# Kernel tuning notes

Hardware: AMD Instinct MI355X
Metric: run time of the kernel (lower is better)

Reference implementation:

```python
import jax, jax.numpy as jnp
import numpy as np

S, B, D = 2048, 2, 768
H = 12
DK = D // H
DFF = 3072
EPS = 1e-5


def _layernorm(x, g, b):
    mu = jnp.mean(x, axis=-1, keepdims=True)
    var = jnp.mean(jnp.square(x - mu), axis=-1, keepdims=True)
    return (x - mu) * jax.lax.rsqrt(var + EPS) * g + b


def setup_inputs() -> dict:
    key = jax.random.key(0)
    ks = jax.random.split(key, 12)
    s = 0.02
    return {
        "x": jax.random.normal(ks[0], (S, B, D), jnp.float32),
        "wq": jax.random.normal(ks[1], (D, D), jnp.float32) * s,
        "bq": jnp.zeros((D,), jnp.float32),
        "wk": jax.random.normal(ks[2], (D, D), jnp.float32) * s,
        "bk": jnp.zeros((D,), jnp.float32),
        "wv": jax.random.normal(ks[3], (D, D), jnp.float32) * s,
        "bv": jnp.zeros((D,), jnp.float32),
        "wo": jax.random.normal(ks[4], (D, D), jnp.float32) * s,
        "bo": jnp.zeros((D,), jnp.float32),
        "g1": jnp.ones((D,), jnp.float32),
        "b1": jnp.zeros((D,), jnp.float32),
        "g2": jnp.ones((D,), jnp.float32),
        "b2": jnp.zeros((D,), jnp.float32),
        "w1": jax.random.normal(ks[5], (DFF, D), jnp.float32) * s,
        "bb1": jnp.zeros((DFF,), jnp.float32),
        "w2": jax.random.normal(ks[6], (D, DFF), jnp.float32) * s,
        "bb2": jnp.zeros((D,), jnp.float32),
    }


def reference(x, wq, bq, wk, bk, wv, bv, wo, bo, g1, b1, g2, b2, w1, bb1, w2, bb2):
    scale = 1.0 / np.sqrt(DK)
    # --- pre-norm MHA ---
    z = _layernorm(x, g1, b1)                      # [S,B,D]
    q = (z @ wq.T + bq).reshape(S, B, H, DK)
    k = (z @ wk.T + bk).reshape(S, B, H, DK)
    v = (z @ wv.T + bv).reshape(S, B, H, DK)
    scores = jnp.einsum('ibhd,jbhd->ijbh', q, k) * scale  # [S,S,B,H]
    attn = jax.nn.softmax(scores, axis=1)                  # softmax over keys
    ctx = jnp.einsum('ijbh,jbhd->ibhd', attn, v).reshape(S, B, D)
    a = ctx @ wo.T + bo
    x = x + a
    # --- pre-norm FFN (ELU) ---
    z = _layernorm(x, g2, b2)
    h = jax.nn.elu(z @ w1.T + bb1)
    a = h @ w2.T + bb2
    return x + a
```

## Files before the change

kernel.cpp:

```cpp
#include <hip/hip_runtime.h>
#include <hip/hip_bf16.h>
#include <math.h>

#define S_LEN   2048
#define B_SZ    2
#define D_MODEL 768
#define N_HEADS 12
#define DFF     3072
#define N_TOK   4096
#define EPS     1e-5f
#define QKV_N   2304
#define SLOG2E  0.18033688011112042f

typedef __attribute__((ext_vector_type(8))) short short8;
typedef __attribute__((ext_vector_type(4))) float f32x4;
typedef unsigned long long u64;
typedef unsigned short u16;
typedef unsigned u32;

__device__ __forceinline__ void gload16(const void* g, void* l) {
    __builtin_amdgcn_global_load_lds(
        (const __attribute__((address_space(1))) void*)g,
        (__attribute__((address_space(3))) void*)l, 16, 0, 0);
}
__device__ __forceinline__ u16 f2bf(float x) {
    union { float f; unsigned u; } c; c.f = x;
    unsigned r = c.u + 0x7FFF + ((c.u >> 16) & 1);
    return (u16)(r >> 16);
}
__device__ __forceinline__ float bf2f(u16 u) {
    union { unsigned u; float f; } c; c.u = ((unsigned)u) << 16; return c.f;
}
__device__ __forceinline__ float fast_exp2(float x) {
    float r; asm("v_exp_f32 %0, %1" : "=v"(r) : "v"(x)); return r;
}

__global__ __launch_bounds__(256) void cvt_all(
    const float* __restrict__ wq, const float* __restrict__ wk,
    const float* __restrict__ wv, const float* __restrict__ wo,
    const float* __restrict__ w1, const float* __restrict__ w2,
    u16* __restrict__ dst)
{
    const int W = 147456;
    int i = blockIdx.x * 256 + threadIdx.x;
    const float* src; int off;
    if      (i <     W) { src = wq; off = 0;     }
    else if (i < 2 * W) { src = wk; off = W;     }
    else if (i < 3 * W) { src = wv; off = 2 * W; }
    else if (i < 4 * W) { src = wo; off = 3 * W; }
    else if (i < 8 * W) { src = w1; off = 4 * W; }
    else                { src = w2; off = 8 * W; }
    float4 v = ((const float4*)src)[i - off];
    union { u16 u[4]; u64 ll; } o;
    o.u[0] = f2bf(v.x); o.u[1] = f2bf(v.y); o.u[2] = f2bf(v.z); o.u[3] = f2bf(v.w);
    ((u64*)dst)[i] = o.ll;
}

__global__ __launch_bounds__(256) void concat_bias(
    const float* __restrict__ bq, const float* __restrict__ bk,
    const float* __restrict__ bv, float* __restrict__ d)
{
    int i = blockIdx.x * 256 + threadIdx.x;
    if (i < 768) d[i] = bq[i];
    else if (i < 1536) d[i] = bk[i - 768];
    else d[i] = bv[i - 1536];
}

__global__ __launch_bounds__(256) void ln_kernel(
    const float* __restrict__ x, const float* __restrict__ g,
    const float* __restrict__ b, u16* __restrict__ z)
{
    int row = blockIdx.x;
    const float* xr = x + (size_t)row * D_MODEL;
    u16* zr = z + (size_t)row * D_MODEL;
    int t = threadIdx.x;
    float loc[3];
    float s1 = 0.f, s2 = 0.f;
#pragma unroll
    for (int i = 0; i < 3; ++i) {
        float v = xr[t + 256 * i];
        loc[i] = v; s1 += v; s2 += v * v;
    }
#pragma unroll
    for (int off = 32; off > 0; off >>= 1) {
        s1 += __shfl_down(s1, off);
        s2 += __shfl_down(s2, off);
    }
    __shared__ float r1[4], r2[4];
    __shared__ float mu_s, is_s;
    int wave = t >> 6, lane = t & 63;
    if (lane == 0) { r1[wave] = s1; r2[wave] = s2; }
    __syncthreads();
    if (t == 0) {
        float a = r1[0] + r1[1] + r1[2] + r1[3];
        float c = r2[0] + r2[1] + r2[2] + r2[3];
        float mu = a * (1.f / D_MODEL);
        float var = c * (1.f / D_MODEL) - mu * mu;
        mu_s = mu; is_s = rsqrtf(var + EPS);
    }
    __syncthreads();
    float mu = mu_s, istd = is_s;
#pragma unroll
    for (int i = 0; i < 3; ++i) {
        int c = t + 256 * i;
        zr[c] = f2bf((loc[i] - mu) * istd * g[c] + b[c]);
    }
}

__global__ __launch_bounds__(256) void ln_fuse(
    const float* __restrict__ x, const u16* __restrict__ p0,
    const u16* __restrict__ p1, const float* __restrict__ bres,
    const float* __restrict__ g, const float* __restrict__ b,
    float* __restrict__ xout, u16* __restrict__ z)
{
    int row = blockIdx.x;
    const float* xr = x + (size_t)row * D_MODEL;
    const u16* p0r = p0 + (size_t)row * D_MODEL;
    const u16* p1r = p1 + (size_t)row * D_MODEL;
    int t = threadIdx.x;
    float loc[3];
    float s1 = 0.f, s2 = 0.f;
#pragma unroll
    for (int i = 0; i < 3; ++i) {
        int c = t + 256 * i;
        float v = xr[c] + bf2f(p0r[c]) + bf2f(p1r[c]) + bres[c];
        loc[i] = v; s1 += v; s2 += v * v;
    }
#pragma unroll
    for (int off = 32; off > 0; off >>= 1) {
        s1 += __shfl_down(s1, off);
        s2 += __shfl_down(s2, off);
    }
    __shared__ float r1[4], r2[4];
    __shared__ float mu_s, is_s;
    int wave = t >> 6, lane = t & 63;
    if (lane == 0) { r1[wave] = s1; r2[wave] = s2; }
    __syncthreads();
    if (t == 0) {
        float a = r1[0] + r1[1] + r1[2] + r1[3];
        float c = r2[0] + r2[1] + r2[2] + r2[3];
        float mu = a * (1.f / D_MODEL);
        float var = c * (1.f / D_MODEL) - mu * mu;
        mu_s = mu; is_s = rsqrtf(var + EPS);
    }
    __syncthreads();
    float mu = mu_s, istd = is_s;
    float* xo = xout + (size_t)row * D_MODEL;
    u16* zr = z + (size_t)row * D_MODEL;
#pragma unroll
    for (int i = 0; i < 3; ++i) {
        int c = t + 256 * i;
        xo[c] = loc[i];
        zr[c] = f2bf((loc[i] - mu) * istd * g[c] + b[c]);
    }
}

template <int MODE>
__global__ __launch_bounds__(256) void gemm_mfma(
    const u16* __restrict__ A, const u16* __restrict__ W,
    const float* __restrict__ bias, void* __restrict__ outp,
    u16* __restrict__ vt, int Ncols, int K, int lda, int ldw, int koff)
{
    __shared__ short AsB[3][128 * 32];
    __shared__ short BsB[3][128 * 32];

    const int t = threadIdx.x;
    const int lane = t & 63, w = t >> 6;
    const int wr = w >> 1, wc = w & 1;
    const int row0 = blockIdx.y * 128, col0 = blockIdx.x * 128;
    const int fr = lane & 15, fg = lane >> 4;

    if (MODE == 4) {
        A += (size_t)blockIdx.z * koff;
        W += (size_t)blockIdx.z * koff;
    }

    int o0 = w * 1024 + lane * 16;
    int r0s = o0 >> 6,          sl0 = (o0 >> 4) & 3;
    int r1s = (o0 + 4096) >> 6, sl1 = ((o0 + 4096) >> 4) & 3;
    int ss0 = sl0 ^ ((r0s >> 1) & 3);
    int ss1 = sl1 ^ ((r1s >> 1) & 3);
    const u16* Asrc0 = A + (size_t)(row0 + r0s) * lda + ss0 * 8;
    const u16* Asrc1 = A + (size_t)(row0 + r1s) * lda + ss1 * 8;
    const u16* Bsrc0 = W + (size_t)(col0 + r0s) * ldw + ss0 * 8;
    const u16* Bsrc1 = W + (size_t)(col0 + r1s) * ldw + ss1 * 8;
    const int od0 = w * 1024, od1 = w * 1024 + 4096;

    f32x4 acc[4][4] = {};
    const int nt = K / 32;

    auto stage = [&](int c, int k0) {
        gload16(Asrc0 + k0, (char*)AsB[c] + od0);
        gload16(Asrc1 + k0, (char*)AsB[c] + od1);
        gload16(Bsrc0 + k0, (char*)BsB[c] + od0);
        gload16(Bsrc1 + k0, (char*)BsB[c] + od1);
    };

    stage(0, 0);
    stage(1, 32);

    for (int tt = 0; tt < nt; ++tt) {
        if (tt + 1 < nt)
            asm volatile("s_waitcnt vmcnt(4)\n\ts_barrier" ::: "memory");
        else
            asm volatile("s_waitcnt vmcnt(0)\n\ts_barrier" ::: "memory");
        if (tt + 2 < nt) stage((tt + 2) % 3, (tt + 2) * 32);

        const char* As = (const char*)AsB[tt % 3];
        const char* Bs = (const char*)BsB[tt % 3];
        short8 af[4], bfr[4];
#pragma unroll
        for (int m = 0; m < 4; ++m) {
            int r = wr * 64 + m * 16 + fr;
            af[m] = *(const short8*)(As + r * 64 + ((fg ^ ((r >> 1) & 3)) << 4));
        }
#pragma unroll
        for (int n = 0; n < 4; ++n) {
            int r = wc * 64 + n * 16 + fr;
            bfr[n] = *(const short8*)(Bs + r * 64 + ((fg ^ ((r >> 1) & 3)) << 4));
        }
#pragma unroll
        for (int m = 0; m < 4; ++m)
#pragma unroll
            for (int n = 0; n < 4; ++n)
                acc[m][n] = __builtin_amdgcn_mfma_f32_16x16x32_bf16(
                    af[m], bfr[n], acc[m][n], 0, 0, 0);
    }

    u16* pout16 = nullptr;
    if (MODE == 4) pout16 = blockIdx.z ? vt : (u16*)outp;

#pragma unroll
    for (int m = 0; m < 4; ++m) {
        int rbase = row0 + wr * 64 + m * 16 + fg * 4;
#pragma unroll
        for (int n = 0; n < 4; ++n) {
            int col = col0 + wc * 64 + n * 16 + fr;
            float bv = (MODE == 4) ? 0.f : bias[col];
            if (MODE == 1 && col >= 1536) {
                int cc = col - 1536, hh = cc >> 6, dk = cc & 63;
                int s_a = rbase >> 1;
                float v0 = acc[m][n][0] + bv, v1 = acc[m][n][1] + bv;
                float v2 = acc[m][n][2] + bv, v3 = acc[m][n][3] + bv;
                unsigned lo = (unsigned)f2bf(v0) | ((unsigned)f2bf(v2) << 16);
                unsigned hi = (unsigned)f2bf(v1) | ((unsigned)f2bf(v3) << 16);
                *(unsigned*)&vt[((size_t)hh * 64 + dk) * 2048 + s_a] = lo;
                *(unsigned*)&vt[((size_t)(N_HEADS + hh) * 64 + dk) * 2048 + s_a] = hi;
            } else {
#pragma unroll
                for (int r = 0; r < 4; ++r) {
                    int row = rbase + r;
                    float v = acc[m][n][r] + bv;
                    if (MODE == 3) {
                        v = v > 0.f ? v : expm1f(v);
                        ((u16*)outp)[(size_t)row * Ncols + col] = f2bf(v);
                    } else if (MODE == 4) {
                        pout16[(size_t)row * 768 + col] = f2bf(v);
                    } else {
                        if (col < 768) v *= SLOG2E;
                        ((u16*)outp)[(size_t)row * QKV_N + col] = f2bf(v);
                    }
                }
            }
        }
    }
}

__global__ __launch_bounds__(256) void reduce_add(
    const u16* __restrict__ p0, const u16* __restrict__ p1,
    const float* __restrict__ bias, const float* __restrict__ res,
    float* __restrict__ out)
{
    int i = blockIdx.x * 256 + threadIdx.x;
    int col4 = i % (D_MODEL / 4);
    u64 a = ((const u64*)p0)[i];
    u64 c = ((const u64*)p1)[i];
    float4 o = ((const float4*)res)[i];
    float4 bb = ((const float4*)bias)[col4];
    o.x += bf2f((u16)a)         + bf2f((u16)c)         + bb.x;
    o.y += bf2f((u16)(a >> 16)) + bf2f((u16)(c >> 16)) + bb.y;
    o.z += bf2f((u16)(a >> 32)) + bf2f((u16)(c >> 32)) + bb.z;
    o.w += bf2f((u16)(a >> 48)) + bf2f((u16)(c >> 48)) + bb.w;
    ((float4*)out)[i] = o;
}

__global__ __launch_bounds__(256) void attn_mfma(
    const u16* __restrict__ qkv, const u16* __restrict__ vt,
    u16* __restrict__ ctx)
{
    __shared__ short KsB[2][64 * 64];
    __shared__ short VtB[2][64 * 64];
    __shared__ short PsB[4][16 * 64];

    const int t = threadIdx.x, lane = t & 63, w = t >> 6;
    const int fr = lane & 15, fg = lane >> 4;
    const int fg4 = fg * 4;
    const int qb = blockIdx.x, bh = blockIdx.y;
    const int b = bh / N_HEADS, h = bh % N_HEADS;

    short8 qf[2];
    {
        int srow = qb * 64 + w * 16 + fr;
        size_t tok = (size_t)srow * B_SZ + b;
#pragma unroll
        for (int s = 0; s < 2; ++s)
            qf[s] = *(const short8*)(qkv + tok * QKV_N + h * 64 + s * 32 + fg * 8);
    }

    const short8 ones8 = { (short)0x3F80, (short)0x3F80, (short)0x3F80, (short)0x3F80,
                           (short)0x3F80, (short)0x3F80, (short)0x3F80, (short)0x3F80 };

    float m2 = -1e30f;
    f32x4 l_acc = {};
    f32x4 O[4] = {};

    int o0 = w * 1024 + lane * 16;
    int r0 = o0 >> 7,          sl0 = (o0 >> 4) & 7;
    int r1 = (o0 + 4096) >> 7, sl1 = ((o0 + 4096) >> 4) & 7;
    int ss0 = sl0 ^ (r0 & 7), ss1 = sl1 ^ (r1 & 7);
    const u16* kbase = qkv + 768 + h * 64;
    const u16* vtb = vt + (size_t)bh * 64 * S_LEN;
    const int od0 = w * 1024, od1 = w * 1024 + 4096;
    char* Pw = (char*)PsB[w];

    auto stageKV = [&](int c, int kb) {
        gload16(kbase + ((size_t)(kb * 64 + r0) * B_SZ + b) * QKV_N + ss0 * 8, (char*)KsB[c] + od0);
        gload16(kbase + ((size_t)(kb * 64 + r1) * B_SZ + b) * QKV_N + ss1 * 8, (char*)KsB[c] + od1);
        gload16(vtb + (size_t)r0 * S_LEN + kb * 64 + ss0 * 8, (char*)VtB[c] + od0);
        gload16(vtb + (size_t)r1 * S_LEN + kb * 64 + ss1 * 8, (char*)VtB[c] + od1);
    };

    stageKV(0, 0);

    for (int kb = 0; kb < S_LEN / 64; ++kb) {
        __syncthreads();
        if (kb + 1 < S_LEN / 64) stageKV((kb + 1) & 1, kb + 1);
        const char* Ks  = (const char*)KsB[kb & 1];
        const char* Vts = (const char*)VtB[kb & 1];

        f32x4 sacc[4] = {};
        __builtin_amdgcn_s_setprio(1);
#pragma unroll
        for (int f = 0; f < 4; ++f) {
            int r = f * 16 + fr;
#pragma unroll
            for (int s = 0; s < 2; ++s) {
                int slot = (s * 4 + fg) ^ (r & 7);
                short8 kf = *(const short8*)(Ks + r * 128 + slot * 16);
                sacc[f] = __builtin_amdgcn_mfma_f32_16x16x32_bf16(kf, qf[s], sacc[f], 0, 0, 0);
            }
        }
        __builtin_amdgcn_s_setprio(0);

        float p[16];
        float mx = -1e30f;
#pragma unroll
        for (int f = 0; f < 4; ++f)
#pragma unroll
            for (int r = 0; r < 4; ++r) {
                float vv = sacc[f][r];
                p[f * 4 + r] = vv;
                mx = fmaxf(mx, vv);
            }
        mx = fmaxf(mx, __shfl_xor(mx, 16));
        mx = fmaxf(mx, __shfl_xor(mx, 32));

        if (!__all(mx - m2 <= 8.f)) {
            float mnew = fmaxf(m2, mx);
            float alpha = fast_exp2(m2 - mnew);
            m2 = mnew;
            float a0 = __shfl(alpha, fg4 + 0), a1 = __shfl(alpha, fg4 + 1);
            float a2 = __shfl(alpha, fg4 + 2), a3 = __shfl(alpha, fg4 + 3);
#pragma unroll
            for (int n = 0; n < 4; ++n) {
                O[n][0] *= a0; O[n][1] *= a1; O[n][2] *= a2; O[n][3] *= a3;
            }
            l_acc[0] *= a0; l_acc[1] *= a1; l_acc[2] *= a2; l_acc[3] *= a3;
        }

#pragma unroll
        for (int i = 0; i < 16; ++i)
            p[i] = fast_exp2(p[i] - m2);

#pragma unroll
        for (int f = 0; f < 4; ++f) {
            u32 u0, u1;
            asm("v_cvt_pk_bf16_f32 %0, %1, %2" : "=v"(u0) : "v"(p[4 * f + 0]), "v"(p[4 * f + 1]));
            asm("v_cvt_pk_bf16_f32 %0, %1, %2" : "=v"(u1) : "v"(p[4 * f + 2]), "v"(p[4 * f + 3]));
            int slot = (f * 2 + (fg >> 1)) ^ (fr & 7);
            uint2 uu; uu.x = u0; uu.y = u1;
            *(uint2*)(Pw + fr * 128 + slot * 16 + (fg & 1) * 8) = uu;
        }
        asm volatile("s_waitcnt lgkmcnt(0)" ::: "memory");
        __builtin_amdgcn_sched_barrier(0);

        __builtin_amdgcn_s_setprio(1);
#pragma unroll
        for (int s = 0; s < 2; ++s) {
            int pslot = (s * 4 + fg) ^ (fr & 7);
            short8 pf = *(const short8*)(Pw + fr * 128 + pslot * 16);
            l_acc = __builtin_amdgcn_mfma_f32_16x16x32_bf16(pf, ones8, l_acc, 0, 0, 0);
#pragma unroll
            for (int n = 0; n < 4; ++n) {
                int vrow = n * 16 + fr;
                int vslot = (s * 4 + fg) ^ (vrow & 7);
                short8 vf = *(const short8*)(Vts + vrow * 128 + vslot * 16);
                O[n] = __builtin_amdgcn_mfma_f32_16x16x32_bf16(pf, vf, O[n], 0, 0, 0);
            }
        }
        __builtin_amdgcn_s_setprio(0);
    }

    float i0 = 1.f / l_acc[0], i1 = 1.f / l_acc[1];
    float i2 = 1.f / l_acc[2], i3 = 1.f / l_acc[3];
    int srow = qb * 64 + w * 16 + fg4;
    size_t tok0 = (size_t)srow * B_SZ + b;
#pragma unroll
    for (int n = 0; n < 4; ++n) {
        int col = h * 64 + n * 16 + fr;
        ctx[(tok0 + 0) * D_MODEL + col] = f2bf(O[n][0] * i0);
        ctx[(tok0 + 2) * D_MODEL + col] = f2bf(O[n][1] * i1);
        ctx[(tok0 + 4) * D_MODEL + col] = f2bf(O[n][2] * i2);
        ctx[(tok0 + 6) * D_MODEL + col] = f2bf(O[n][3] * i3);
    }
}

extern "C" void kernel_launch(void* const* d_in, const int* in_sizes, int n_in,
                              void* d_out, int out_size, void* d_ws, size_t ws_size,
                              hipStream_t stream)
{
    (void)in_sizes; (void)n_in; (void)out_size; (void)ws_size;
    const float* x   = (const float*)d_in[0];
    const float* wq  = (const float*)d_in[1];
    const float* bq  = (const float*)d_in[2];
    const float* wk  = (const float*)d_in[3];
    const float* bk  = (const float*)d_in[4];
    const float* wv  = (const float*)d_in[5];
    const float* bv  = (const float*)d_in[6];
    const float* wo  = (const float*)d_in[7];
    const float* bo  = (const float*)d_in[8];
    const float* g1  = (const float*)d_in[9];
    const float* b1  = (const float*)d_in[10];
    const float* g2  = (const float*)d_in[11];
    const float* b2  = (const float*)d_in[12];
    const float* w1  = (const float*)d_in[13];
    const float* bb1 = (const float*)d_in[14];
    const float* w2  = (const float*)d_in[15];
    const float* bb2 = (const float*)d_in[16];
    float* out = (float*)d_out;

    const size_t ND = (size_t)N_TOK * D_MODEL;
    char* p = (char*)d_ws;
    u16* z    = (u16*)p;
    p += ND * 2;
    u16* qkv  = (u16*)p;
    u16* hbuf = (u16*)p;
    p += (size_t)N_TOK * QKV_N * 2;
    u16* vtb  = (u16*)p;
    p += (size_t)B_SZ * N_HEADS * 64 * S_LEN * 2;
    u16* wqkvb = (u16*)p;
    p += (size_t)QKV_N * D_MODEL * 2;
    u16* wob   = (u16*)p; p += (size_t)D_MODEL * D_MODEL * 2;
    u16* w1b   = (u16*)p; p += (size_t)DFF * D_MODEL * 2;
    u16* w2b   = (u16*)p; p += (size_t)D_MODEL * DFF * 2;
    float* biasqkv = (float*)p;

    u16* wop0 = qkv;
    u16* wop1 = qkv + ND;
    u16* fp0  = z;
    u16* fp1  = wqkvb;

    dim3 blk(256);

    cvt_all<<<6912, blk, 0, stream>>>(wq, wk, wv, wo, w1, w2, wqkvb);
    concat_bias<<<9, blk, 0, stream>>>(bq, bk, bv, biasqkv);

    ln_kernel<<<N_TOK, blk, 0, stream>>>(x, g1, b1, z);
    gemm_mfma<1><<<dim3(QKV_N / 128, N_TOK / 128), blk, 0, stream>>>(
        z, wqkvb, biasqkv, qkv, vtb, QKV_N, D_MODEL, D_MODEL, D_MODEL, 0);
    attn_mfma<<<dim3(S_LEN / 64, B_SZ * N_HEADS), blk, 0, stream>>>(qkv, vtb, z);
    gemm_mfma<4><<<dim3(D_MODEL / 128, N_TOK / 128, 2), blk, 0, stream>>>(
        z, wob, nullptr, wop0, wop1, D_MODEL, 384, D_MODEL, D_MODEL, 384);
    ln_fuse<<<N_TOK, blk, 0, stream>>>(x, wop0, wop1, bo, g2, b2, out, z);
    gemm_mfma<3><<<dim3(DFF / 128, N_TOK / 128), blk, 0, stream>>>(
        z, w1b, bb1, hbuf, nullptr, DFF, D_MODEL, D_MODEL, D_MODEL, 0);
    gemm_mfma<4><<<dim3(D_MODEL / 128, N_TOK / 128, 2), blk, 0, stream>>>(
        hbuf, w2b, nullptr, fp0, fp1, D_MODEL, 1536, DFF, DFF, 1536);
    reduce_add<<<(int)(ND / 4 / 256), blk, 0, stream>>>(fp0, fp1, bb2, out, out);
}
```

Measured before the change: 202.6 us.

## Split attention over key dimension with separate combine kernel; fast ELU exp

Attention now runs with a grid z-dimension of two, each half handling half of the key tiles and writing unnormalized bf16 partial outputs plus per-row max and sum into reused workspace. A new combine kernel merges the two partials with log-sum-exp rescaling into the context buffer. The aim is to double the number of blocks (768 instead of 384), improving CU occupancy on the many-CU GPU. In exchange it adds an extra launch, extra memory traffic, and bf16 rounding of unnormalized partials. Separately, the ELU's expm1f is replaced by fast_exp2 minus one, which loses accuracy near zero.

New measurement: 202.5 us. No clear change (-0.1%).

```diff
diff --git a/kernel.cpp b/kernel.cpp
--- a/kernel.cpp
+++ b/kernel.cpp
@@ -11,6 +11,8 @@
 #define EPS     1e-5f
 #define QKV_N   2304
 #define SLOG2E  0.18033688011112042f
+#define NSPLIT  2
+#define NTILE   (S_LEN / 64 / NSPLIT)
 
 typedef __attribute__((ext_vector_type(8))) short short8;
 typedef __attribute__((ext_vector_type(4))) float f32x4;
@@ -252,7 +254,7 @@
                     int row = rbase + r;
                     float v = acc[m][n][r] + bv;
                     if (MODE == 3) {
-                        v = v > 0.f ? v : expm1f(v);
+                        v = v > 0.f ? v : (fast_exp2(v * 1.44269504f) - 1.f);
                         ((u16*)outp)[(size_t)row * Ncols + col] = f2bf(v);
                     } else if (MODE == 4) {
                         pout16[(size_t)row * 768 + col] = f2bf(v);
@@ -285,8 +287,8 @@
 }
 
 __global__ __launch_bounds__(256) void attn_mfma(
-    const u16* __restrict__ qkv, const u16* __restrict__ vt,
-    u16* __restrict__ ctx)
+    const u16* qkv, const u16* __restrict__ vt,
+    u16* op0, u16* __restrict__ op1, float2* __restrict__ mlp)
 {
     __shared__ short KsB[2][64 * 64];
     __shared__ short VtB[2][64 * 64];
@@ -295,7 +297,7 @@
     const int t = threadIdx.x, lane = t & 63, w = t >> 6;
     const int fr = lane & 15, fg = lane >> 4;
     const int fg4 = fg * 4;
-    const int qb = blockIdx.x, bh = blockIdx.y;
+    const int qb = blockIdx.x, bh = blockIdx.y, zid = blockIdx.z;
     const int b = bh / N_HEADS, h = bh % N_HEADS;
 
     short8 qf[2];
@@ -330,13 +332,14 @@
         gload16(vtb + (size_t)r1 * S_LEN + kb * 64 + ss1 * 8, (char*)VtB[c] + od1);
     };
 
-    stageKV(0, 0);
-
-    for (int kb = 0; kb < S_LEN / 64; ++kb) {
+    const int kb0 = zid * NTILE;
+    stageKV(0, kb0);
+
+    for (int it = 0; it < NTILE; ++it) {
         __syncthreads();
-        if (kb + 1 < S_LEN / 64) stageKV((kb + 1) & 1, kb + 1);
-        const char* Ks  = (const char*)KsB[kb & 1];
-        const char* Vts = (const char*)VtB[kb & 1];
+        if (it + 1 < NTILE) stageKV((it + 1) & 1, kb0 + it + 1);
+        const char* Ks  = (const char*)KsB[it & 1];
+        const char* Vts = (const char*)VtB[it & 1];
 
         f32x4 sacc[4] = {};
         __builtin_amdgcn_s_setprio(1);
@@ -411,18 +414,49 @@
         __builtin_amdgcn_s_setprio(0);
     }
 
-    float i0 = 1.f / l_acc[0], i1 = 1.f / l_acc[1];
-    float i2 = 1.f / l_acc[2], i3 = 1.f / l_acc[3];
+    float mm0 = __shfl(m2, fg4 + 0), mm1 = __shfl(m2, fg4 + 1);
+    float mm2 = __shfl(m2, fg4 + 2), mm3 = __shfl(m2, fg4 + 3);
     int srow = qb * 64 + w * 16 + fg4;
     size_t tok0 = (size_t)srow * B_SZ + b;
+    u16* op = zid ? op1 : op0;
+    const int ld = zid ? 768 : QKV_N;
 #pragma unroll
     for (int n = 0; n < 4; ++n) {
         int col = h * 64 + n * 16 + fr;
-        ctx[(tok0 + 0) * D_MODEL + col] = f2bf(O[n][0] * i0);
-        ctx[(tok0 + 2) * D_MODEL + col] = f2bf(O[n][1] * i1);
-        ctx[(tok0 + 4) * D_MODEL + col] = f2bf(O[n][2] * i2);
-        ctx[(tok0 + 6) * D_MODEL + col] = f2bf(O[n][3] * i3);
-    }
+        op[(tok0 + 0) * ld + col] = f2bf(O[n][0]);
+        op[(tok0 + 2) * ld + col] = f2bf(O[n][1]);
+        op[(tok0 + 4) * ld + col] = f2bf(O[n][2]);
+        op[(tok0 + 6) * ld + col] = f2bf(O[n][3]);
+    }
+    if (fr == 0) {
+        float2* mlz = mlp + (size_t)zid * (N_TOK * N_HEADS);
+        mlz[(tok0 + 0) * N_HEADS + h] = make_float2(mm0, l_acc[0]);
+        mlz[(tok0 + 2) * N_HEADS + h] = make_float2(mm1, l_acc[1]);
+        mlz[(tok0 + 4) * N_HEADS + h] = make_float2(mm2, l_acc[2]);
+        mlz[(tok0 + 6) * N_HEADS + h] = make_float2(mm3, l_acc[3]);
+    }
+}
+
+__global__ __launch_bounds__(256) void combine_attn(
+    const u16* __restrict__ op0, const u16* op1,
+    const float2* __restrict__ ml, u16* ctx)
+{
+    int i = blockIdx.x * 256 + threadIdx.x;
+    int tok = i / 192, c4 = i % 192, h = c4 >> 4;
+    float2 q0 = ml[tok * N_HEADS + h];
+    float2 q1 = ml[N_TOK * N_HEADS + tok * N_HEADS + h];
+    float m = fmaxf(q0.x, q1.x);
+    float a0 = fast_exp2(q0.x - m), a1 = fast_exp2(q1.x - m);
+    float inv = 1.f / (a0 * q0.y + a1 * q1.y);
+    a0 *= inv; a1 *= inv;
+    u64 o0 = *(const u64*)(op0 + (size_t)tok * QKV_N + c4 * 4);
+    u64 o1 = *(const u64*)(op1 + (size_t)tok * 768 + c4 * 4);
+    union { u16 u[4]; u64 ll; } r;
+#pragma unroll
+    for (int j = 0; j < 4; ++j)
+        r.u[j] = f2bf(a0 * bf2f((u16)(o0 >> (16 * j))) +
+                      a1 * bf2f((u16)(o1 >> (16 * j))));
+    *(u64*)(ctx + (size_t)tok * 768 + c4 * 4) = r.ll;
 }
 
 extern "C" void kernel_launch(void* const* d_in, const int* in_sizes, int n_in,
@@ -465,6 +499,9 @@
     u16* w2b   = (u16*)p; p += (size_t)D_MODEL * DFF * 2;
     float* biasqkv = (float*)p;
 
+    u16* aop0 = qkv + 1536;
+    u16* aop1 = z;
+    float2* aml = (float2*)wqkvb;
     u16* wop0 = qkv;
     u16* wop1 = qkv + ND;
     u16* fp0  = z;
@@ -478,7 +515,9 @@
     ln_kernel<<<N_TOK, blk, 0, stream>>>(x, g1, b1, z);
     gemm_mfma<1><<<dim3(QKV_N / 128, N_TOK / 128), blk, 0, stream>>>(
         z, wqkvb, biasqkv, qkv, vtb, QKV_N, D_MODEL, D_MODEL, D_MODEL, 0);
-    attn_mfma<<<dim3(S_LEN / 64, B_SZ * N_HEADS), blk, 0, stream>>>(qkv, vtb, z);
+    attn_mfma<<<dim3(S_LEN / 64, B_SZ * N_HEADS, NSPLIT), blk, 0, stream>>>(
+        qkv, vtb, aop0, aop1, aml);
+    combine_attn<<<(int)(ND / 4 / 256), blk, 0, stream>>>(aop0, aop1, aml, z);
     gemm_mfma<4><<<dim3(D_MODEL / 128, N_TOK / 128, 2), blk, 0, stream>>>(
         z, wob, nullptr, wop0, wop1, D_MODEL, 384, D_MODEL, D_MODEL, 384);
     ln_fuse<<<N_TOK, blk, 0, stream>>>(x, wop0, wop1, bo, g2, b2, out, z);
```
